# Optimization experiments

Measured on AMD Instinct MI355X. Metric: run time of the kernel, lower is better.

Reference implementation:

```python
import jax, jax.numpy as jnp
import numpy as np

N = 50000          # num nodes
E_RAND = 600000    # random edges (self-loops appended -> E = E_RAND + N)
HEADS = 4
OUT_CH = 16
OUT_NEURONS = 2 * OUT_CH   # diag reparam: [mean | std-logit]
IN_CH = 128
NEG_SLOPE = 0.2


def setup_inputs() -> dict:
    key = jax.random.key(0)
    k1, k2, k3, k4, k5 = jax.random.split(key, 5)
    x = jax.random.normal(k1, (N, IN_CH), jnp.float32)
    src = jax.random.randint(k2, (E_RAND,), 0, N, jnp.int32)
    dst = jax.random.randint(k3, (E_RAND,), 0, N, jnp.int32)
    loops = jnp.arange(N, dtype=jnp.int32)
    edge_index = jnp.stack([jnp.concatenate([src, loops]),
                            jnp.concatenate([dst, loops])])  # [2, E]
    # glorot init for weight [IN_CH, HEADS*OUT_NEURONS]
    s_w = float(np.sqrt(6.0 / (IN_CH + HEADS * OUT_NEURONS)))
    weight = jax.random.uniform(k4, (IN_CH, HEADS * OUT_NEURONS), jnp.float32, -s_w, s_w)
    # glorot for att [1, HEADS, 2*OUT_NEURONS]
    s_a = float(np.sqrt(6.0 / (HEADS + 2 * OUT_NEURONS)))
    att = jax.random.uniform(k5, (1, HEADS, 2 * OUT_NEURONS), jnp.float32, -s_a, s_a)
    bias = jnp.zeros((HEADS * OUT_NEURONS,), jnp.float32)
    return {"x": x, "edge_index": edge_index, "weight": weight, "att": att, "bias": bias}


def reference(x, edge_index, weight, att, bias):
    src, dst = edge_index[0], edge_index[1]  # j -> i (PyG source_to_target)
    h = (x @ weight).reshape(N, HEADS, OUT_NEURONS)          # Theta x
    x_j = h[src]                                             # [E, H, On]
    x_i = h[dst]                                             # [E, H, On]
    # alpha = LeakyReLU(a^T [x_i || x_j])
    alpha = (x_i * att[:, :, :OUT_NEURONS]).sum(-1) + \
            (x_j * att[:, :, OUT_NEURONS:]).sum(-1)          # [E, H]
    alpha = jax.nn.leaky_relu(alpha, NEG_SLOPE)
    # segment softmax over neighborhoods of target node i
    m = jax.ops.segment_max(alpha, dst, num_segments=N)      # [N, H]
    e = jnp.exp(alpha - m[dst])
    denom = jax.ops.segment_sum(e, dst, num_segments=N)      # [N, H]
    alpha = e / (denom[dst] + 1e-16)                          # [E, H]
    # scatter-add aggregation of attention-weighted features
    agg = jax.ops.segment_sum(x_j * alpha[:, :, None], dst, num_segments=N)  # [N, H, On]
    out = agg.reshape(N, HEADS * OUT_NEURONS) + bias
    # VIB diag reparameterization + closed-form KL against N(0, I)
    o = out.reshape(N * HEADS, OUT_NEURONS)
    mean = o[:, :OUT_CH]
    std = jax.nn.softplus(o[:, OUT_CH:] - 5.0) + 1e-10
    kl = (-jnp.log(std) + 0.5 * (std * std + mean * mean) - 0.5).sum(-1)  # [N*H]
    ixz = kl.reshape(N, HEADS).mean(-1)                      # [N]
    # eval + val_use_mean=True: output is the mean part
    out_final = mean.reshape(N, HEADS * OUT_CH)
    structure_kl_loss = jnp.zeros((), jnp.float32)
    return out_final, ixz, structure_kl_loss, mean, std
```

## Files before the change

### kernel.cpp

```cpp
#include <hip/hip_runtime.h>
#include <stdint.h>

#define NN 50000
#define NB 196
#define NEG_SLOPE 0.2f
#define WTS 136

#define IXZ_OFF    (NN * 64)
#define SKL_OFF    (NN * 64 + NN)
#define MEAN_OFF   (NN * 64 + NN + 1)
#define STD_OFF    (MEAN_OFF + NN * 64)

typedef unsigned int u32;
typedef unsigned short u16;
typedef __attribute__((ext_vector_type(8))) short short8;
typedef __attribute__((ext_vector_type(4))) float f32x4;

__device__ __forceinline__ float bf2f(u16 s) { return __uint_as_float(((u32)s) << 16); }
__device__ __forceinline__ u16 f2bf(float f) {
    u32 u = __float_as_uint(f);
    u += 0x7FFFu + ((u >> 16) & 1u);
    return (u16)(u >> 16);
}
__device__ __forceinline__ float lo16(u32 u) { return __uint_as_float(u << 16); }
__device__ __forceinline__ float hi16(u32 u) { return __uint_as_float(u & 0xFFFF0000u); }
__device__ __forceinline__ float softplusf(float x) {
    return fmaxf(x, 0.f) + log1pf(expf(-fabsf(x)));
}
__device__ __forceinline__ void stout(void* o, long long idx, float v, bool f32) {
    if (f32) ((float*)o)[idx] = v;
    else     ((u16*)o)[idx]   = f2bf(v);
}
__device__ __forceinline__ int wscan_incl(int v, int lane) {
#pragma unroll
    for (int off = 1; off < 64; off <<= 1) {
        int u = __shfl_up(v, off);
        if (lane >= off) v += u;
    }
    return v;
}

__global__ __launch_bounds__(256) void k_wt(const u32* __restrict__ xw,
                                            const void* __restrict__ wv_,
                                            int* __restrict__ flag,
                                            u16* __restrict__ wtg,
                                            int* __restrict__ zbase)
{
    __shared__ int lflag;
    const int t = threadIdx.x;
    if (t < 64) {
        u32 wrd = xw[t];
        u32 e = (wrd >> 7) & 0xFF;
        bool plaus = (e >= 0x60 && e <= 0x85);
        unsigned long long b = __ballot(plaus);
        if (t == 0) {
            int f = (__popcll(b) < 32) ? 1 : 0;
            lflag = f;
            if (blockIdx.x == 0) flag[0] = f;
        }
    }
    __syncthreads();
    const bool f32 = lflag != 0;

    const int gid = blockIdx.x * 256 + t;
    for (int i = gid; i < 2 * NN; i += 8 * 256) zbase[i] = 0;

    const int k = blockIdx.x * 16 + (t >> 4);
    const int cq = t & 15;
    u16 v[8];
    if (f32) {
        const float* w = (const float*)wv_;
        float4 a = *(const float4*)(w + k * 128 + cq * 8);
        float4 b = *(const float4*)(w + k * 128 + cq * 8 + 4);
        v[0] = f2bf(a.x); v[1] = f2bf(a.y); v[2] = f2bf(a.z); v[3] = f2bf(a.w);
        v[4] = f2bf(b.x); v[5] = f2bf(b.y); v[6] = f2bf(b.z); v[7] = f2bf(b.w);
    } else {
        const u16* w = (const u16*)wv_;
        uint4 u = *(const uint4*)(w + k * 128 + cq * 8);
        v[0] = (u16)(u.x & 0xFFFF); v[1] = (u16)(u.x >> 16);
        v[2] = (u16)(u.y & 0xFFFF); v[3] = (u16)(u.y >> 16);
        v[4] = (u16)(u.z & 0xFFFF); v[5] = (u16)(u.z >> 16);
        v[6] = (u16)(u.w & 0xFFFF); v[7] = (u16)(u.w >> 16);
    }
#pragma unroll
    for (int j = 0; j < 8; j++)
        wtg[(cq * 8 + j) * WTS + k] = v[j];
}

__global__ __launch_bounds__(256) void k_gemm(
    const void* __restrict__ xv, const u16* __restrict__ wtg,
    const void* __restrict__ attv, const int* __restrict__ flag,
    u16* __restrict__ hb, float* __restrict__ ai, float* __restrict__ aj,
    const int* __restrict__ dst, int* __restrict__ counts, int E)
{
    __shared__ __align__(16) u16 ls[128 * WTS];
    const int tid = threadIdx.x;
    const bool f32 = flag[0] != 0;

    {
        uint4* d = (uint4*)ls;
        const uint4* s = (const uint4*)wtg;
        for (int i = tid; i < 128 * WTS / 8; i += 256) d[i] = s[i];
    }

    const int w = tid >> 6, L = tid & 63;
    const int q = L >> 4, c15 = L & 15;
    const int nb16 = blockIdx.x * 64 + w * 16;

    short8 afr[4];
    {
        int nrow = nb16 + c15; if (nrow > NN - 1) nrow = NN - 1;
        if (f32) {
            const float* xp = (const float*)xv + (size_t)nrow * 128 + q * 8;
#pragma unroll
            for (int ks = 0; ks < 4; ks++) {
                float4 a = *(const float4*)(xp + ks * 32);
                float4 b = *(const float4*)(xp + ks * 32 + 4);
                union { short8 s; u16 e[8]; } u;
                u.e[0] = f2bf(a.x); u.e[1] = f2bf(a.y); u.e[2] = f2bf(a.z); u.e[3] = f2bf(a.w);
                u.e[4] = f2bf(b.x); u.e[5] = f2bf(b.y); u.e[6] = f2bf(b.z); u.e[7] = f2bf(b.w);
                afr[ks] = u.s;
            }
        } else {
            const u16* xp = (const u16*)xv + (size_t)nrow * 128 + q * 8;
#pragma unroll
            for (int ks = 0; ks < 4; ks++)
                afr[ks] = *(const short8*)(xp + ks * 32);
        }
    }
    __syncthreads();

    f32x4 acc[8];
#pragma unroll
    for (int t = 0; t < 8; t++) {
        acc[t] = (f32x4){0.f, 0.f, 0.f, 0.f};
        const u16* bp = ls + (16 * t + c15) * WTS + q * 8;
#pragma unroll
        for (int ks = 0; ks < 4; ks++) {
            short8 bfr = *(const short8*)(bp + ks * 32);
            acc[t] = __builtin_amdgcn_mfma_f32_16x16x32_bf16(afr[ks], bfr, acc[t], 0, 0, 0);
        }
    }

    float ati[8], atj[8];
#pragma unroll
    for (int t = 0; t < 8; t++) {
        int p = (t >> 1) * 64 + (t & 1) * 16 + c15;
        if (f32) {
            ati[t] = ((const float*)attv)[p];
            atj[t] = ((const float*)attv)[p + 32];
        } else {
            ati[t] = bf2f(((const u16*)attv)[p]);
            atj[t] = bf2f(((const u16*)attv)[p + 32]);
        }
    }
#pragma unroll
    for (int r = 0; r < 4; r++) {
        int node = nb16 + q * 4 + r;
#pragma unroll
        for (int h = 0; h < 4; h++) {
            float pi = acc[2 * h][r] * ati[2 * h] + acc[2 * h + 1][r] * ati[2 * h + 1];
            float pj = acc[2 * h][r] * atj[2 * h] + acc[2 * h + 1][r] * atj[2 * h + 1];
            pi += __shfl_xor(pi, 1); pj += __shfl_xor(pj, 1);
            pi += __shfl_xor(pi, 2); pj += __shfl_xor(pj, 2);
            pi += __shfl_xor(pi, 4); pj += __shfl_xor(pj, 4);
            pi += __shfl_xor(pi, 8); pj += __shfl_xor(pj, 8);
            if (c15 == 0 && node < NN) { ai[node * 4 + h] = pi; aj[node * 4 + h] = pj; }
        }
    }

    __syncthreads();
    u16* myls = ls + w * 16 * WTS;
#pragma unroll
    for (int t = 0; t < 8; t++)
#pragma unroll
        for (int r = 0; r < 4; r++)
            myls[(q * 4 + r) * WTS + 16 * t + c15] = f2bf(acc[t][r]);
#pragma unroll
    for (int v = 0; v < 4; v++) {
        int idx = v * 64 + L;
        int nrow = idx >> 4, c8 = idx & 15;
        int node = nb16 + nrow;
        if (node < NN)
            *(uint4*)(hb + (size_t)node * 128 + c8 * 8) =
                *(const uint4*)(myls + nrow * WTS + c8 * 8);
    }

    const int gid = blockIdx.x * 256 + tid;
    const int stride = gridDim.x * 256;
    for (int e = gid; e < E; e += stride)
        atomicAdd(&counts[dst[e]], 1);
}

__global__ __launch_bounds__(256) void k_scan1(const int* __restrict__ counts,
                                               int* __restrict__ lexcl,
                                               int* __restrict__ blocksum)
{
    __shared__ int wsum[4];
    const int t = threadIdx.x, lane = t & 63, wv = t >> 6;
    const int i = blockIdx.x * 256 + t;
    int c = (i < NN) ? counts[i] : 0;
    int inc = wscan_incl(c, lane);
    if (lane == 63) wsum[wv] = inc;
    __syncthreads();
    int add = 0;
#pragma unroll
    for (int k = 0; k < 3; k++) if (k < wv) add += wsum[k];
    inc += add;
    if (i < NN) lexcl[i] = inc - c;
    if (t == 255) blocksum[blockIdx.x] = inc;
}

__global__ __launch_bounds__(256) void k_scan2(const int* __restrict__ blocksum,
                                               int* __restrict__ blockoff)
{
    __shared__ int wsum[4];
    const int t = threadIdx.x, lane = t & 63, wv = t >> 6;
    int c = (t < NB) ? blocksum[t] : 0;
    int inc = wscan_incl(c, lane);
    if (lane == 63) wsum[wv] = inc;
    __syncthreads();
    int add = 0;
#pragma unroll
    for (int k = 0; k < 3; k++) if (k < wv) add += wsum[k];
    inc += add;
    if (t < NB) blockoff[t] = inc - c;
}

__global__ __launch_bounds__(256) void k_fill(
    const int* __restrict__ src, const int* __restrict__ dst,
    const int* __restrict__ lexcl, const int* __restrict__ blockoff,
    int* __restrict__ cursor, int* __restrict__ perm_src, int E)
{
    int e = blockIdx.x * 256 + threadIdx.x;
    if (e >= E) return;
    int d = dst[e];
    int pos = blockoff[d >> 8] + lexcl[d] + atomicAdd(&cursor[d], 1);
    perm_src[pos] = src[e];
}

__global__ __launch_bounds__(256) void k_agg(
    const int* __restrict__ lexcl, const int* __restrict__ blockoff,
    const int* __restrict__ counts, const int* __restrict__ perm_src,
    const float* __restrict__ ai, const float* __restrict__ aj,
    const u16* __restrict__ hb, const void* __restrict__ biasv,
    const int* __restrict__ flag, void* __restrict__ outv)
{
    const int t = blockIdx.x * 256 + threadIdx.x;
    const int node = t >> 4;
    if (node >= NN) return;
    const bool f32 = flag[0] != 0;
    const int l = t & 15;
    const int head = l >> 2;
    const int cc0 = (l & 3) << 3;

    const int rs = blockoff[node >> 8] + lexcl[node];
    const int re = rs + counts[node];
    const float ain = ai[node * 4 + head];
    const u16* hl8 = hb + l * 8;

    float dsum = 0.f;
    float a0 = 0.f, a1 = 0.f, a2 = 0.f, a3 = 0.f;
    float a4 = 0.f, a5 = 0.f, a6 = 0.f, a7 = 0.f;

    int i = rs;
    for (; i + 1 < re; i += 2) {
        int s0 = perm_src[i], s1 = perm_src[i + 1];
        float x0 = aj[s0 * 4 + head] + ain;
        float x1 = aj[s1 * 4 + head] + ain;
        x0 = x0 > 0.f ? x0 : NEG_SLOPE * x0;
        x1 = x1 > 0.f ? x1 : NEG_SLOPE * x1;
        float e0 = __expf(x0), e1 = __expf(x1);
        uint4 h0 = *(const uint4*)(hl8 + (size_t)s0 * 128);
        uint4 h1 = *(const uint4*)(hl8 + (size_t)s1 * 128);
        dsum += e0 + e1;
        a0 += e0 * lo16(h0.x) + e1 * lo16(h1.x);
        a1 += e0 * hi16(h0.x) + e1 * hi16(h1.x);
        a2 += e0 * lo16(h0.y) + e1 * lo16(h1.y);
        a3 += e0 * hi16(h0.y) + e1 * hi16(h1.y);
        a4 += e0 * lo16(h0.z) + e1 * lo16(h1.z);
        a5 += e0 * hi16(h0.z) + e1 * hi16(h1.z);
        a6 += e0 * lo16(h0.w) + e1 * lo16(h1.w);
        a7 += e0 * hi16(h0.w) + e1 * hi16(h1.w);
    }
    if (i < re) {
        int s0 = perm_src[i];
        float x0 = aj[s0 * 4 + head] + ain;
        x0 = x0 > 0.f ? x0 : NEG_SLOPE * x0;
        float e0 = __expf(x0);
        uint4 h0 = *(const uint4*)(hl8 + (size_t)s0 * 128);
        dsum += e0;
        a0 += e0 * lo16(h0.x); a1 += e0 * hi16(h0.x);
        a2 += e0 * lo16(h0.y); a3 += e0 * hi16(h0.y);
        a4 += e0 * lo16(h0.z); a5 += e0 * hi16(h0.z);
        a6 += e0 * lo16(h0.w); a7 += e0 * hi16(h0.w);
    }

    const float inv = 1.f / (dsum + 1e-16f);
    const int cb = head * 32 + cc0;
    float v[8];
    if (f32) {
        const float* bias = (const float*)biasv;
#pragma unroll
        for (int j = 0; j < 8; j++) v[j] = bias[cb + j];
    } else {
        const u16* bias = (const u16*)biasv;
#pragma unroll
        for (int j = 0; j < 8; j++) v[j] = bf2f(bias[cb + j]);
    }
    v[0] += a0 * inv; v[1] += a1 * inv; v[2] += a2 * inv; v[3] += a3 * inv;
    v[4] += a4 * inv; v[5] += a5 * inv; v[6] += a6 * inv; v[7] += a7 * inv;

    float part = 0.f;
    if (cc0 < 16) {
#pragma unroll
        for (int j = 0; j < 8; j++) part += 0.5f * v[j] * v[j];
        long long o = (long long)node * 64 + head * 16 + cc0;
#pragma unroll
        for (int j = 0; j < 8; j++) stout(outv, o + j, v[j], f32);
        long long om = (long long)MEAN_OFF + o;
#pragma unroll
        for (int j = 0; j < 8; j++) stout(outv, om + j, v[j], f32);
    } else {
        long long os = (long long)STD_OFF + (long long)node * 64 + head * 16 + (cc0 - 16);
#pragma unroll
        for (int j = 0; j < 8; j++) {
            float s = softplusf(v[j] - 5.f) + 1e-10f;
            part += -logf(s) + 0.5f * s * s - 0.5f;
            stout(outv, os + j, s, f32);
        }
    }
    part += __shfl_xor(part, 1); part += __shfl_xor(part, 2);
    part += __shfl_xor(part, 4); part += __shfl_xor(part, 8);
    if (l == 0) stout(outv, (long long)IXZ_OFF + node, part * 0.25f, f32);
    if (t == 0) stout(outv, (long long)SKL_OFF, 0.f, f32);
}

extern "C" void kernel_launch(void* const* d_in, const int* in_sizes, int n_in,
                              void* d_out, int out_size, void* d_ws, size_t ws_size,
                              hipStream_t stream)
{
    const void* x    = d_in[0];
    const int*  ei   = (const int*)d_in[1];
    const void* w    = d_in[2];
    const void* att  = d_in[3];
    const void* bias = d_in[4];

    const int E = in_sizes[1] / 2;
    const int* src = ei;
    const int* dst = ei + E;

    u16*   hb        = (u16*)d_ws;
    float* ai        = (float*)(hb + (size_t)NN * 128);
    float* aj        = ai + NN * 4;
    int*   perm_src  = (int*)(aj + NN * 4);
    int*   counts    = perm_src + E;
    int*   cursor    = counts + NN;
    int*   lexcl     = cursor + NN;
    int*   blocksum  = lexcl + NN;
    int*   blockoff  = blocksum + NB;
    int*   flag      = blockoff + NB;
    u16*   wtg       = (u16*)(flag + 1);

    k_wt<<<8, 256, 0, stream>>>((const u32*)x, w, flag, wtg, counts);
    k_gemm<<<(NN + 63) / 64, 256, 0, stream>>>(x, wtg, att, flag, hb, ai, aj,
                                               dst, counts, E);
    k_scan1<<<NB, 256, 0, stream>>>(counts, lexcl, blocksum);
    k_scan2<<<1, 256, 0, stream>>>(blocksum, blockoff);
    k_fill<<<(E + 255) / 256, 256, 0, stream>>>(src, dst, lexcl, blockoff,
                                                cursor, perm_src, E);
    k_agg<<<(NN * 16 + 255) / 256, 256, 0, stream>>>(lexcl, blockoff, counts,
                                                     perm_src, ai, aj, hb, bias,
                                                     flag, d_out);
}
```

Baseline: 210.0 us.

## Store projected features in fp8, fuse scan kernels, detect dtype per block

The projected node features are now stored as fp8 (e4m3) instead of bf16, which halves the bytes gathered per edge in the aggregation kernel. The two-level scan is merged into one kernel: the last block to finish, found with an atomic counter, computes the block offsets. The global dtype flag is dropped in favour of per-block detection, and the zeroing of counts is spread over 64 blocks. FP8 storage costs accuracy in the aggregated mean and std outputs and may exceed the tolerance.

```diff
diff --git a/kernel.cpp b/kernel.cpp
--- a/kernel.cpp
+++ b/kernel.cpp
@@ -3,6 +3,7 @@
 
 #define NN 50000
 #define NB 196
+#define NTILES 782
 #define NEG_SLOPE 0.2f
 #define WTS 136
 
@@ -13,8 +14,10 @@
 
 typedef unsigned int u32;
 typedef unsigned short u16;
+typedef unsigned char u8;
 typedef __attribute__((ext_vector_type(8))) short short8;
 typedef __attribute__((ext_vector_type(4))) float f32x4;
+typedef __attribute__((ext_vector_type(2))) float f32x2;
 
 __device__ __forceinline__ float bf2f(u16 s) { return __uint_as_float(((u32)s) << 16); }
 __device__ __forceinline__ u16 f2bf(float f) {
@@ -40,62 +43,67 @@
     return v;
 }
 
-__global__ __launch_bounds__(256) void k_wt(const u32* __restrict__ xw,
-                                            const void* __restrict__ wv_,
-                                            int* __restrict__ flag,
-                                            u16* __restrict__ wtg,
-                                            int* __restrict__ zbase)
-{
-    __shared__ int lflag;
+__device__ __forceinline__ bool detect_f32_block(const u32* __restrict__ xw,
+                                                 int* lflag)
+{
     const int t = threadIdx.x;
     if (t < 64) {
         u32 wrd = xw[t];
         u32 e = (wrd >> 7) & 0xFF;
         bool plaus = (e >= 0x60 && e <= 0x85);
         unsigned long long b = __ballot(plaus);
-        if (t == 0) {
-            int f = (__popcll(b) < 32) ? 1 : 0;
-            lflag = f;
-            if (blockIdx.x == 0) flag[0] = f;
-        }
+        if (t == 0) *lflag = (__popcll(b) < 32) ? 1 : 0;
     }
     __syncthreads();
-    const bool f32 = lflag != 0;
-
-    const int gid = blockIdx.x * 256 + t;
-    for (int i = gid; i < 2 * NN; i += 8 * 256) zbase[i] = 0;
-
-    const int k = blockIdx.x * 16 + (t >> 4);
-    const int cq = t & 15;
-    u16 v[8];
-    if (f32) {
-        const float* w = (const float*)wv_;
-        float4 a = *(const float4*)(w + k * 128 + cq * 8);
-        float4 b = *(const float4*)(w + k * 128 + cq * 8 + 4);
-        v[0] = f2bf(a.x); v[1] = f2bf(a.y); v[2] = f2bf(a.z); v[3] = f2bf(a.w);
-        v[4] = f2bf(b.x); v[5] = f2bf(b.y); v[6] = f2bf(b.z); v[7] = f2bf(b.w);
-    } else {
-        const u16* w = (const u16*)wv_;
-        uint4 u = *(const uint4*)(w + k * 128 + cq * 8);
-        v[0] = (u16)(u.x & 0xFFFF); v[1] = (u16)(u.x >> 16);
-        v[2] = (u16)(u.y & 0xFFFF); v[3] = (u16)(u.y >> 16);
-        v[4] = (u16)(u.z & 0xFFFF); v[5] = (u16)(u.z >> 16);
-        v[6] = (u16)(u.w & 0xFFFF); v[7] = (u16)(u.w >> 16);
-    }
-#pragma unroll
-    for (int j = 0; j < 8; j++)
-        wtg[(cq * 8 + j) * WTS + k] = v[j];
+    return *lflag != 0;
+}
+
+__global__ __launch_bounds__(256) void k_wt(const void* __restrict__ xv,
+                                            const void* __restrict__ wv_,
+                                            u16* __restrict__ wtg,
+                                            int* __restrict__ zbase)
+{
+    __shared__ int lflag;
+    const bool f32 = detect_f32_block((const u32*)xv, &lflag);
+    const int t = threadIdx.x;
+
+    for (int i = blockIdx.x * 256 + t; i < 2 * NN + 1; i += 64 * 256)
+        zbase[i] = 0;
+
+    if (blockIdx.x < 8) {
+        const int k = blockIdx.x * 16 + (t >> 4);
+        const int cq = t & 15;
+        u16 v[8];
+        if (f32) {
+            const float* w = (const float*)wv_;
+            float4 a = *(const float4*)(w + k * 128 + cq * 8);
+            float4 b = *(const float4*)(w + k * 128 + cq * 8 + 4);
+            v[0] = f2bf(a.x); v[1] = f2bf(a.y); v[2] = f2bf(a.z); v[3] = f2bf(a.w);
+            v[4] = f2bf(b.x); v[5] = f2bf(b.y); v[6] = f2bf(b.z); v[7] = f2bf(b.w);
+        } else {
+            const u16* w = (const u16*)wv_;
+            uint4 u = *(const uint4*)(w + k * 128 + cq * 8);
+            v[0] = (u16)(u.x & 0xFFFF); v[1] = (u16)(u.x >> 16);
+            v[2] = (u16)(u.y & 0xFFFF); v[3] = (u16)(u.y >> 16);
+            v[4] = (u16)(u.z & 0xFFFF); v[5] = (u16)(u.z >> 16);
+            v[6] = (u16)(u.w & 0xFFFF); v[7] = (u16)(u.w >> 16);
+        }
+#pragma unroll
+        for (int j = 0; j < 8; j++)
+            wtg[(cq * 8 + j) * WTS + k] = v[j];
+    }
 }
 
 __global__ __launch_bounds__(256) void k_gemm(
     const void* __restrict__ xv, const u16* __restrict__ wtg,
-    const void* __restrict__ attv, const int* __restrict__ flag,
-    u16* __restrict__ hb, float* __restrict__ ai, float* __restrict__ aj,
+    const void* __restrict__ attv, u8* __restrict__ hb,
+    float* __restrict__ ai, float* __restrict__ aj,
     const int* __restrict__ dst, int* __restrict__ counts, int E)
 {
     __shared__ __align__(16) u16 ls[128 * WTS];
+    __shared__ int lflag;
+    const bool f32 = detect_f32_block((const u32*)xv, &lflag);
     const int tid = threadIdx.x;
-    const bool f32 = flag[0] != 0;
 
     {
         uint4* d = (uint4*)ls;
@@ -181,9 +189,20 @@
         int idx = v * 64 + L;
         int nrow = idx >> 4, c8 = idx & 15;
         int node = nb16 + nrow;
-        if (node < NN)
-            *(uint4*)(hb + (size_t)node * 128 + c8 * 8) =
-                *(const uint4*)(myls + nrow * WTS + c8 * 8);
+        uint4 t16 = *(const uint4*)(myls + nrow * WTS + c8 * 8);
+        float f0 = lo16(t16.x), f1 = hi16(t16.x);
+        float f2 = lo16(t16.y), f3 = hi16(t16.y);
+        float f4 = lo16(t16.z), f5 = hi16(t16.z);
+        float f6 = lo16(t16.w), f7 = hi16(t16.w);
+        u32 lo = 0, hi = 0;
+        lo = __builtin_amdgcn_cvt_pk_fp8_f32(f0, f1, lo, false);
+        lo = __builtin_amdgcn_cvt_pk_fp8_f32(f2, f3, lo, true);
+        hi = __builtin_amdgcn_cvt_pk_fp8_f32(f4, f5, hi, false);
+        hi = __builtin_amdgcn_cvt_pk_fp8_f32(f6, f7, hi, true);
+        if (node < NN) {
+            uint2 o; o.x = lo; o.y = hi;
+            *(uint2*)(hb + (size_t)node * 128 + c8 * 8) = o;
+        }
     }
 
     const int gid = blockIdx.x * 256 + tid;
@@ -194,9 +213,13 @@
 
 __global__ __launch_bounds__(256) void k_scan1(const int* __restrict__ counts,
                                                int* __restrict__ lexcl,
-                                               int* __restrict__ blocksum)
+                                               int* __restrict__ blocksum,
+                                               int* __restrict__ done,
+                                               int* __restrict__ sboff_g)
 {
     __shared__ int wsum[4];
+    __shared__ int sboff[256];
+    __shared__ int lastf;
     const int t = threadIdx.x, lane = t & 63, wv = t >> 6;
     const int i = blockIdx.x * 256 + t;
     int c = (i < NN) ? counts[i] : 0;
@@ -208,56 +231,58 @@
     for (int k = 0; k < 3; k++) if (k < wv) add += wsum[k];
     inc += add;
     if (i < NN) lexcl[i] = inc - c;
-    if (t == 255) blocksum[blockIdx.x] = inc;
-}
-
-__global__ __launch_bounds__(256) void k_scan2(const int* __restrict__ blocksum,
-                                               int* __restrict__ blockoff)
-{
-    __shared__ int wsum[4];
-    const int t = threadIdx.x, lane = t & 63, wv = t >> 6;
-    int c = (t < NB) ? blocksum[t] : 0;
-    int inc = wscan_incl(c, lane);
-    if (lane == 63) wsum[wv] = inc;
+    if (t == 255) {
+        blocksum[blockIdx.x] = inc;
+        __threadfence();
+        lastf = (atomicAdd(done, 1) == NB - 1) ? 1 : 0;
+    }
     __syncthreads();
-    int add = 0;
-#pragma unroll
-    for (int k = 0; k < 3; k++) if (k < wv) add += wsum[k];
-    inc += add;
-    if (t < NB) blockoff[t] = inc - c;
+    if (lastf) {
+        __threadfence();
+        int c2 = (t < NB) ? blocksum[t] : 0;
+        int inc2 = wscan_incl(c2, lane);
+        if (lane == 63) wsum[wv] = inc2;
+        __syncthreads();
+        int add2 = 0;
+#pragma unroll
+        for (int k = 0; k < 3; k++) if (k < wv) add2 += wsum[k];
+        sboff[t] = inc2 + add2 - c2;
+        __syncthreads();
+        sboff_g[t] = sboff[t];
+    }
 }
 
 __global__ __launch_bounds__(256) void k_fill(
-    const int* __restrict__ src, const int* __restrict__ dst,
-    const int* __restrict__ lexcl, const int* __restrict__ blockoff,
-    int* __restrict__ cursor, int* __restrict__ perm_src, int E)
+    const int* __restrict__ ei, const int* __restrict__ lexcl,
+    const int* __restrict__ sboff_g, int* __restrict__ cursor,
+    int* __restrict__ perm_src, int E)
 {
     int e = blockIdx.x * 256 + threadIdx.x;
     if (e >= E) return;
-    int d = dst[e];
-    int pos = blockoff[d >> 8] + lexcl[d] + atomicAdd(&cursor[d], 1);
-    perm_src[pos] = src[e];
+    int d = ei[E + e];
+    int pos = sboff_g[d >> 8] + lexcl[d] + atomicAdd(&cursor[d], 1);
+    perm_src[pos] = ei[e];
 }
 
 __global__ __launch_bounds__(256) void k_agg(
-    const int* __restrict__ lexcl, const int* __restrict__ blockoff,
+    const int* __restrict__ lexcl, const int* __restrict__ sboff_g,
     const int* __restrict__ counts, const int* __restrict__ perm_src,
     const float* __restrict__ ai, const float* __restrict__ aj,
-    const u16* __restrict__ hb, const void* __restrict__ biasv,
-    const int* __restrict__ flag, void* __restrict__ outv)
-{
+    const u8* __restrict__ hb, const void* __restrict__ biasv,
+    const void* __restrict__ xv, void* __restrict__ outv)
+{
+    __shared__ int lflag;
+    const bool f32 = detect_f32_block((const u32*)xv, &lflag);
     const int t = blockIdx.x * 256 + threadIdx.x;
     const int node = t >> 4;
-    if (node >= NN) return;
-    const bool f32 = flag[0] != 0;
     const int l = t & 15;
     const int head = l >> 2;
     const int cc0 = (l & 3) << 3;
 
-    const int rs = blockoff[node >> 8] + lexcl[node];
+    const int rs = sboff_g[node >> 8] + lexcl[node];
     const int re = rs + counts[node];
     const float ain = ai[node * 4 + head];
-    const u16* hl8 = hb + l * 8;
+    const u8* hl8 = hb + l * 8;
 
     float dsum = 0.f;
     float a0 = 0.f, a1 = 0.f, a2 = 0.f, a3 = 0.f;
@@ -271,29 +296,37 @@
         x0 = x0 > 0.f ? x0 : NEG_SLOPE * x0;
         x1 = x1 > 0.f ? x1 : NEG_SLOPE * x1;
         float e0 = __expf(x0), e1 = __expf(x1);
-        uint4 h0 = *(const uint4*)(hl8 + (size_t)s0 * 128);
-        uint4 h1 = *(const uint4*)(hl8 + (size_t)s1 * 128);
+        uint2 h0 = *(const uint2*)(hl8 + (size_t)s0 * 128);
+        uint2 h1 = *(const uint2*)(hl8 + (size_t)s1 * 128);
+        f32x2 p0 = __builtin_amdgcn_cvt_pk_f32_fp8(h0.x, false);
+        f32x2 p1 = __builtin_amdgcn_cvt_pk_f32_fp8(h0.x, true);
+        f32x2 p2 = __builtin_amdgcn_cvt_pk_f32_fp8(h0.y, false);
+        f32x2 p3 = __builtin_amdgcn_cvt_pk_f32_fp8(h0.y, true);
+        f32x2 q0 = __builtin_amdgcn_cvt_pk_f32_fp8(h1.x, false);
+        f32x2 q1 = __builtin_amdgcn_cvt_pk_f32_fp8(h1.x, true);
+        f32x2 q2 = __builtin_amdgcn_cvt_pk_f32_fp8(h1.y, false);
+        f32x2 q3 = __builtin_amdgcn_cvt_pk_f32_fp8(h1.y, true);
         dsum += e0 + e1;
-        a0 += e0 * lo16(h0.x) + e1 * lo16(h1.x);
-        a1 += e0 * hi16(h0.x) + e1 * hi16(h1.x);
-        a2 += e0 * lo16(h0.y) + e1 * lo16(h1.y);
-        a3 += e0 * hi16(h0.y) + e1 * hi16(h1.y);
-        a4 += e0 * lo16(h0.z) + e1 * lo16(h1.z);
-        a5 += e0 * hi16(h0.z) + e1 * hi16(h1.z);
-        a6 += e0 * lo16(h0.w) + e1 * lo16(h1.w);
-        a7 += e0 * hi16(h0.w) + e1 * hi16(h1.w);
+        a0 += e0 * p0.x + e1 * q0.x;  a1 += e0 * p0.y + e1 * q0.y;
+        a2 += e0 * p1.x + e1 * q1.x;  a3 += e0 * p1.y + e1 * q1.y;
+        a4 += e0 * p2.x + e1 * q2.x;  a5 += e0 * p2.y + e1 * q2.y;
+        a6 += e0 * p3.x + e1 * q3.x;  a7 += e0 * p3.y + e1 * q3.y;
     }
     if (i < re) {
         int s0 = perm_src[i];
         float x0 = aj[s0 * 4 + head] + ain;
         x0 = x0 > 0.f ? x0 : NEG_SLOPE * x0;
         float e0 = __expf(x0);
-        uint4 h0 = *(const uint4*)(hl8 + (size_t)s0 * 128);
+        uint2 h0 = *(const uint2*)(hl8 + (size_t)s0 * 128);
+        f32x2 p0 = __builtin_amdgcn_cvt_pk_f32_fp8(h0.x, false);
+        f32x2 p1 = __builtin_amdgcn_cvt_pk_f32_fp8(h0.x, true);
+        f32x2 p2 = __builtin_amdgcn_cvt_pk_f32_fp8(h0.y, false);
+        f32x2 p3 = __builtin_amdgcn_cvt_pk_f32_fp8(h0.y, true);
         dsum += e0;
-        a0 += e0 * lo16(h0.x); a1 += e0 * hi16(h0.x);
-        a2 += e0 * lo16(h0.y); a3 += e0 * hi16(h0.y);
-        a4 += e0 * lo16(h0.z); a5 += e0 * hi16(h0.z);
-        a6 += e0 * lo16(h0.w); a7 += e0 * hi16(h0.w);
+        a0 += e0 * p0.x; a1 += e0 * p0.y;
+        a2 += e0 * p1.x; a3 += e0 * p1.y;
+        a4 += e0 * p2.x; a5 += e0 * p2.y;
+        a6 += e0 * p3.x; a7 += e0 * p3.y;
     }
 
     const float inv = 1.f / (dsum + 1e-16f);
@@ -345,31 +378,27 @@
     const void* w    = d_in[2];
     const void* att  = d_in[3];
     const void* bias = d_in[4];
-
-    const int E = in_sizes[1] / 2;
-    const int* src = ei;
-    const int* dst = ei + E;
-
-    u16*   hb        = (u16*)d_ws;
-    float* ai        = (float*)(hb + (size_t)NN * 128);
-    float* aj        = ai + NN * 4;
-    int*   perm_src  = (int*)(aj + NN * 4);
-    int*   counts    = perm_src + E;
-    int*   cursor    = counts + NN;
-    int*   lexcl     = cursor + NN;
-    int*   blocksum  = lexcl + NN;
-    int*   blockoff  = blocksum + NB;
-    int*   flag      = blockoff + NB;
-    u16*   wtg       = (u16*)(flag + 1);
-
-    k_wt<<<8, 256, 0, stream>>>((const u32*)x, w, flag, wtg, counts);
-    k_gemm<<<(NN + 63) / 64, 256, 0, stream>>>(x, wtg, att, flag, hb, ai, aj,
-                                               dst, counts, E);
-    k_scan1<<<NB, 256, 0, stream>>>(counts, lexcl, blocksum);
-    k_scan2<<<1, 256, 0, stream>>>(blocksum, blockoff);
-    k_fill<<<(E + 255) / 256, 256, 0, stream>>>(src, dst, lexcl, blockoff,
+    int E = in_sizes[1] / 2;
+
+    u8*    hb       = (u8*)d_ws;
+    float* ai       = (float*)(hb + (size_t)NN * 128);
+    float* aj       = ai + NN * 4;
+    int*   perm_src = (int*)(aj + NN * 4);
+    int*   counts   = perm_src + E;
+    int*   cursor   = counts + NN;
+    int*   done     = cursor + NN;
+    int*   lexcl    = done + 1;
+    int*   blocksum = lexcl + NN;
+    int*   sboff_g  = blocksum + NB;
+    u16*   wtg      = (u16*)(((uintptr_t)(sboff_g + 256) + 15) & ~(uintptr_t)15);
+
+    k_wt<<<64, 256, 0, stream>>>(x, w, wtg, counts);
+    k_gemm<<<NTILES, 256, 0, stream>>>(x, wtg, att, hb, ai, aj,
+                                       ei + E, counts, E);
+    k_scan1<<<NB, 256, 0, stream>>>(counts, lexcl, blocksum, done, sboff_g);
+    k_fill<<<(E + 255) / 256, 256, 0, stream>>>(ei, lexcl, sboff_g,
                                                 cursor, perm_src, E);
-    k_agg<<<(NN * 16 + 255) / 256, 256, 0, stream>>>(lexcl, blockoff, counts,
-                                                     perm_src, ai, aj, hb, bias,
-                                                     flag, d_out);
-}
+    k_agg<<<(NN * 16) / 256, 256, 0, stream>>>(lexcl, sboff_g, counts,
+                                               perm_src, ai, aj, hb,
+                                               bias, x, d_out);
+}
```

Result: no change. 208.2 us (-0.8%).
